# Kernel optimization log

Measured on AMD Instinct MI355X. Metric: run time of the kernel, lower is better.

## Reference

```python
import jax, jax.numpy as jnp
import numpy as np

B, C, H, W = 4, 512, 64, 208
HID = 512          # params.text_hidden_dim; must equal C for view(1,C,H,-1)
DS = 16            # 1/scale_factor for nearest downsample of the mask
N_REG = 4          # four region-indexed attention modules


def setup_inputs() -> dict:
    key = jax.random.key(0)
    ks = jax.random.split(key, 7)
    image_feature = jax.random.normal(ks[0], (B, C, H, W), dtype=jnp.float32)
    text_feat = jax.random.normal(ks[1], (N_REG, B, HID), dtype=jnp.float32)
    # Mask is constant per (full-res) column so that each region's pixel count
    # is divisible by H, as the original view(1, C, H, -1) requires.
    col_labels = jax.random.randint(ks[2], (B, W * DS), 1, N_REG + 1)
    text_mask = jnp.broadcast_to(
        col_labels[:, None, None, :], (B, 1, H * DS, W * DS)
    ).astype(jnp.int32)
    # Per-region MHA params (nn.Linear weights, no bias assumed).
    Wq = jax.random.normal(ks[3], (N_REG, C, HID), dtype=jnp.float32) * (C ** -0.5)
    Wk = jax.random.normal(ks[4], (N_REG, HID, HID), dtype=jnp.float32) * (HID ** -0.5)
    Wv = jax.random.normal(ks[5], (N_REG, HID, HID), dtype=jnp.float32) * (HID ** -0.5)
    Wo = jax.random.normal(ks[6], (N_REG, HID, C), dtype=jnp.float32) * (HID ** -0.5)
    return {
        "image_feature": image_feature,
        "text_feat": text_feat,
        "text_mask": text_mask,
        "Wq": Wq,
        "Wk": Wk,
        "Wv": Wv,
        "Wo": Wo,
    }


def reference(image_feature, text_feat, text_mask, Wq, Wk, Wv, Wo):
    # F.interpolate(scale=1/16, mode='nearest') == strided slicing for integer stride.
    mask_ds = text_mask[:, 0, ::DS, ::DS]          # [B, H, W]
    col_labels = mask_ds[:, 0, :]                  # [B, W] (mask is column-constant)
    # Cross-attention of every region pixel (query) against ONE text token z
    # (single key/value): softmax over a length-1 axis is identically 1, so
    # attn_out = Wo @ (Wv @ z) for every pixel, and Wq/Wk receive zero gradient.
    # With the residual connection: out_pixel = x_pixel + (z Wv) Wo per region.
    delta = jnp.einsum('rbh,rhd,rdc->brc', text_feat, Wv, Wo)          # [B, R, C]
    d_col = jnp.take_along_axis(delta, (col_labels - 1)[:, :, None], axis=1)  # [B, W, C]
    out = image_feature + d_col.transpose(0, 2, 1)[:, :, None, :]      # [B, C, H, W]
    # The torch code concatenates regions along width in sorted-unique label
    # order, i.e. columns are permuted by (label, original column) -- a stable
    # argsort of the column labels.
    order = jnp.argsort(col_labels, axis=1, stable=True)               # [B, W]
    return jnp.take_along_axis(out, order[:, None, None, :], axis=3)
```

## Files before the change

### kernel.cpp

```cpp
#include <hip/hip_runtime.h>

#define B_ 4
#define C_ 512
#define H_ 64
#define W_ 208
#define HID_ 512
#define NREG_ 4
#define DS_ 16


__global__ __launch_bounds__(256) void prepA_kernel(
    const float* __restrict__ tf, const float* __restrict__ Wv,
    const int* __restrict__ mask, float* __restrict__ tmp, int* __restrict__ swl) {
  int blk = blockIdx.x, tid = threadIdx.x;
  if (blk < 256) {
    int r = blk >> 6;
    int h0 = ((blk >> 3) & 7) * 64;
    int d0 = (blk & 7) * 64;
    int g = tid >> 6, dd = tid & 63;
    __shared__ float tf_s[B_][64];
    __shared__ float red[4][B_][64];
    tf_s[g][dd] = tf[(r * B_ + g) * HID_ + h0 + dd];
    __syncthreads();
    float acc[B_] = {};
    for (int hh = g * 16; hh < g * 16 + 16; ++hh) {
      float w = Wv[(size_t)(r * HID_ + h0 + hh) * HID_ + d0 + dd];
#pragma unroll
      for (int b = 0; b < B_; ++b) acc[b] += tf_s[b][hh] * w;
    }
#pragma unroll
    for (int b = 0; b < B_; ++b) red[g][b][dd] = acc[b];
    __syncthreads();
    {
      float s = red[0][g][dd] + red[1][g][dd] + red[2][g][dd] + red[3][g][dd];
      atomicAdd(&tmp[(g * NREG_ + r) * HID_ + d0 + dd], s);
    }
  } else {
    int b = blk - 256;
    const size_t mb = (size_t)b * (H_ * DS_) * (W_ * DS_);
    int w = tid;
    int l = (w < W_) ? (mask[mb + (size_t)w * DS_] - 1) : -1;
    int wave = tid >> 6, lane = tid & 63;
    unsigned long long bal[NREG_];
    __shared__ int wcnt[4][NREG_];
#pragma unroll
    for (int r = 0; r < NREG_; ++r) bal[r] = __ballot(l == r);
    if (lane < NREG_) wcnt[wave][lane] = __popcll(bal[lane]);
    __syncthreads();
    if (w < W_) {
      int pos = 0;
#pragma unroll
      for (int q = 0; q < NREG_; ++q) {
        int tot = wcnt[0][q] + wcnt[1][q] + wcnt[2][q] + wcnt[3][q];
        if (q < l) pos += tot;
      }
#pragma unroll
      for (int v = 0; v < 4; ++v)
        if (v < wave) pos += wcnt[v][l];
      pos += __popcll(bal[l] & ((1ull << lane) - 1ull));
      swl[b * W_ + pos] = w | (l << 16);
    }
  }
}

__global__ __launch_bounds__(256) void prepB_kernel(
    const float* __restrict__ tmp, const float* __restrict__ Wo,
    float* __restrict__ delta) {
  int blk = blockIdx.x, tid = threadIdx.x;
  int r = blk >> 6;
  int d0 = ((blk >> 3) & 7) * 64;
  int c0 = (blk & 7) * 64;
  int g = tid >> 6, cc = tid & 63;
  __shared__ float tmp_s[B_][64];
  __shared__ float red[4][B_][64];
  tmp_s[g][cc] = tmp[(g * NREG_ + r) * HID_ + d0 + cc];
  __syncthreads();
  float acc[B_] = {};
  for (int dd = g * 16; dd < g * 16 + 16; ++dd) {
    float w = Wo[(size_t)(r * HID_ + d0 + dd) * C_ + c0 + cc];
#pragma unroll
    for (int b = 0; b < B_; ++b) acc[b] += tmp_s[b][dd] * w;
  }
#pragma unroll
  for (int b = 0; b < B_; ++b) red[g][b][cc] = acc[b];
  __syncthreads();
  {
    float s = red[0][g][cc] + red[1][g][cc] + red[2][g][cc] + red[3][g][cc];
    atomicAdd(&delta[(g * NREG_ + r) * C_ + c0 + cc], s);
  }
}

#define GITER_ 13
#define RCH_ (W_ / 4)
__global__ void apply_kernel(
    const float* __restrict__ img, const float* __restrict__ delta,
    const int* __restrict__ swl, float* __restrict__ out) {
  int blk = blockIdx.x;
  int b = blk >> 9;
  int c = blk & (C_ - 1);
  int tid = threadIdx.x;
  __shared__ int swl_s[W_];
  __shared__ float dsel_s[NREG_];
  if (tid < W_) swl_s[tid] = swl[b * W_ + tid];
  if (tid < NREG_) dsel_s[tid] = delta[(b * NREG_ + tid) * C_ + c];
  __syncthreads();
  float d0 = dsel_s[0], d1 = dsel_s[1], d2 = dsel_s[2], d3 = dsel_s[3];
  const float* src = img + (size_t)blk * (H_ * W_);
  float4* dst = (float4*)(out + (size_t)blk * (H_ * W_));
  float res[GITER_][4];
#pragma unroll
  for (int g = 0; g < GITER_; ++g) {
    int i = g * 256 + tid;
    int h = i / RCH_;
    int j = i - h * RCH_;
    const float* row = src + h * W_;
#pragma unroll
    for (int k = 0; k < 4; ++k)
      res[g][k] = row[swl_s[j * 4 + k] & 0xFFFF];
  }
#pragma unroll
  for (int g = 0; g < GITER_; ++g) {
    int i = g * 256 + tid;
    int h = i / RCH_;
    int j = i - h * RCH_;
    float4 o;
    float* op = &o.x;
#pragma unroll
    for (int k = 0; k < 4; ++k) {
      int r = swl_s[j * 4 + k] >> 16;
      float dv = (r == 0) ? d0 : (r == 1) ? d1 : (r == 2) ? d2 : d3;
      op[k] = res[g][k] + dv;
    }
    dst[i] = o;
  }
}

extern "C" void kernel_launch(void* const* d_in, const int* in_sizes, int n_in,
                              void* d_out, int out_size, void* d_ws, size_t ws_size,
                              hipStream_t stream) {
  const float* img  = (const float*)d_in[0];
  const float* tf   = (const float*)d_in[1];
  const int*   mask = (const int*)d_in[2];
  const float* Wv   = (const float*)d_in[5];
  const float* Wo   = (const float*)d_in[6];
  float* delta = (float*)d_ws;
  float* tmp   = (float*)((char*)d_ws + 32768);
  int*   swl   = (int*)((char*)d_ws + 65536);
  float* out   = (float*)d_out;

  hipMemsetAsync(d_ws, 0, 65536, stream);
  prepA_kernel<<<260, 256, 0, stream>>>(tf, Wv, mask, tmp, swl);
  prepB_kernel<<<256, 256, 0, stream>>>(tmp, Wo, delta);
  apply_kernel<<<B_ * C_, 256, 0, stream>>>(img, delta, swl, out);
}
```

Before: 237.2 us.

## Stage image rows in LDS for coalesced loads and permute from shared memory

The apply kernel now loads 16-row tiles of the image with coalesced float4 reads, adds a per-column delta that is precomputed into shared memory, writes the result to an LDS tile, and then performs the column permutation as a gather from LDS before coalesced float4 stores. This replaces scattered scalar global gathers and the per-element region select. It adds extra barriers per tile, about 13KB of LDS per block, and a launch-bounds occupancy hint.

```diff
diff --git a/kernel.cpp b/kernel.cpp
--- a/kernel.cpp
+++ b/kernel.cpp
@@ -90,48 +90,64 @@
   }
 }
 
-#define GITER_ 13
 #define RCH_ (W_ / 4)
-__global__ void apply_kernel(
+#define TROWS_ 16
+#define TF4_ (TROWS_ * RCH_)
+__global__ __launch_bounds__(256, 8) void apply_kernel(
     const float* __restrict__ img, const float* __restrict__ delta,
     const int* __restrict__ swl, float* __restrict__ out) {
   int blk = blockIdx.x;
   int b = blk >> 9;
-  int c = blk & (C_ - 1);
   int tid = threadIdx.x;
   __shared__ int swl_s[W_];
+  __shared__ float dval[W_];
   __shared__ float dsel_s[NREG_];
+  __shared__ float tile[TROWS_ * W_];
   if (tid < W_) swl_s[tid] = swl[b * W_ + tid];
-  if (tid < NREG_) dsel_s[tid] = delta[(b * NREG_ + tid) * C_ + c];
+  if (tid < NREG_) dsel_s[tid] = delta[(b * NREG_ + tid) * C_ + (blk & (C_ - 1))];
   __syncthreads();
-  float d0 = dsel_s[0], d1 = dsel_s[1], d2 = dsel_s[2], d3 = dsel_s[3];
-  const float* src = img + (size_t)blk * (H_ * W_);
-  float4* dst = (float4*)(out + (size_t)blk * (H_ * W_));
-  float res[GITER_][4];
+  if (tid < W_) {
+    int e = swl_s[tid];
+    dval[e & 0xFFFF] = dsel_s[e >> 16];
+  }
+  __syncthreads();
+  const float4* srcv = (const float4*)(img + (size_t)blk * (H_ * W_));
+  float4* dstv = (float4*)(out + (size_t)blk * (H_ * W_));
+  const float4* dval4 = (const float4*)dval;
+  const int4* swl4 = (const int4*)swl_s;
+  for (int t = 0; t < H_ / TROWS_; ++t) {
+    int base = t * TF4_;
 #pragma unroll
-  for (int g = 0; g < GITER_; ++g) {
-    int i = g * 256 + tid;
-    int h = i / RCH_;
-    int j = i - h * RCH_;
-    const float* row = src + h * W_;
+    for (int g = 0; g < 4; ++g) {
+      int ii = g * 256 + tid;
+      if (ii < TF4_) {
+        float4 v = srcv[base + ii];
+        int hl = ii / RCH_;
+        int j = ii - hl * RCH_;
+        float4 dv = dval4[j];
+        float4 o;
+        o.x = v.x + dv.x; o.y = v.y + dv.y; o.z = v.z + dv.z; o.w = v.w + dv.w;
+        ((float4*)&tile[hl * W_])[j] = o;
+      }
+    }
+    __syncthreads();
 #pragma unroll
-    for (int k = 0; k < 4; ++k)
-      res[g][k] = row[swl_s[j * 4 + k] & 0xFFFF];
-  }
-#pragma unroll
-  for (int g = 0; g < GITER_; ++g) {
-    int i = g * 256 + tid;
-    int h = i / RCH_;
-    int j = i - h * RCH_;
-    float4 o;
-    float* op = &o.x;
-#pragma unroll
-    for (int k = 0; k < 4; ++k) {
-      int r = swl_s[j * 4 + k] >> 16;
-      float dv = (r == 0) ? d0 : (r == 1) ? d1 : (r == 2) ? d2 : d3;
-      op[k] = res[g][k] + dv;
+    for (int g = 0; g < 4; ++g) {
+      int ii = g * 256 + tid;
+      if (ii < TF4_) {
+        int hl = ii / RCH_;
+        int jo = ii - hl * RCH_;
+        int4 sw = swl4[jo];
+        const float* rowp = &tile[hl * W_];
+        float4 o;
+        o.x = rowp[sw.x & 0xFFFF];
+        o.y = rowp[sw.y & 0xFFFF];
+        o.z = rowp[sw.z & 0xFFFF];
+        o.w = rowp[sw.w & 0xFFFF];
+        dstv[base + ii] = o;
+      }
     }
-    dst[i] = o;
+    __syncthreads();
   }
 }
 
```

Result: slower. 245.3 us (+3.4%).

## Stage image rows in LDS with coalesced float4 loads, drop memset and atomics

Applied to the files above, without the earlier changes.

The apply kernel now has each wave load its 16-row slab of the image with coalesced float4 reads into registers, write it to shared memory, and do the column permutation gather from LDS. This replaces the scattered per-element global reads. Per-column deltas are precomputed into a shared array. The two GEMV prep kernels are restructured so each block covers the full reduction dimension and writes results directly, which removes the memset and the atomicAdds at the cost of fewer, longer-running blocks. The new 53KB LDS tile may limit occupancy in the apply kernel.

```diff
diff --git a/kernel.cpp b/kernel.cpp
--- a/kernel.cpp
+++ b/kernel.cpp
@@ -9,34 +9,42 @@
 #define DS_ 16
 
 
-__global__ __launch_bounds__(256) void prepA_kernel(
+__global__ __launch_bounds__(256) void prep1_kernel(
     const float* __restrict__ tf, const float* __restrict__ Wv,
     const int* __restrict__ mask, float* __restrict__ tmp, int* __restrict__ swl) {
   int blk = blockIdx.x, tid = threadIdx.x;
-  if (blk < 256) {
-    int r = blk >> 6;
-    int h0 = ((blk >> 3) & 7) * 64;
-    int d0 = (blk & 7) * 64;
-    int g = tid >> 6, dd = tid & 63;
-    __shared__ float tf_s[B_][64];
-    __shared__ float red[4][B_][64];
-    tf_s[g][dd] = tf[(r * B_ + g) * HID_ + h0 + dd];
+  if (blk < 64) {
+    int r = blk >> 4;
+    int d0 = (blk & 15) * 32;
+    __shared__ float tf_s[B_ * HID_];
+    __shared__ float red[8][B_][32];
+#pragma unroll
+    for (int k = 0; k < 8; ++k) {
+      int idx = k * 256 + tid;
+      tf_s[idx] = tf[r * (B_ * HID_) + idx];
+    }
     __syncthreads();
+    int hg = tid >> 5, dd = tid & 31;
     float acc[B_] = {};
-    for (int hh = g * 16; hh < g * 16 + 16; ++hh) {
-      float w = Wv[(size_t)(r * HID_ + h0 + hh) * HID_ + d0 + dd];
+#pragma unroll 4
+    for (int q = 0; q < 64; ++q) {
+      int hh = hg * 64 + q;
+      float w = Wv[(size_t)(r * HID_ + hh) * HID_ + d0 + dd];
 #pragma unroll
-      for (int b = 0; b < B_; ++b) acc[b] += tf_s[b][hh] * w;
+      for (int b = 0; b < B_; ++b) acc[b] += tf_s[b * HID_ + hh] * w;
     }
 #pragma unroll
-    for (int b = 0; b < B_; ++b) red[g][b][dd] = acc[b];
+    for (int b = 0; b < B_; ++b) red[hg][b][dd] = acc[b];
     __syncthreads();
-    {
-      float s = red[0][g][dd] + red[1][g][dd] + red[2][g][dd] + red[3][g][dd];
-      atomicAdd(&tmp[(g * NREG_ + r) * HID_ + d0 + dd], s);
+    if (tid < 128) {
+      int b2 = tid >> 5, d2 = tid & 31;
+      float s = 0.f;
+#pragma unroll
+      for (int q = 0; q < 8; ++q) s += red[q][b2][d2];
+      tmp[(b2 * NREG_ + r) * HID_ + d0 + d2] = s;
     }
   } else {
-    int b = blk - 256;
+    int b = blk - 64;
     const size_t mb = (size_t)b * (H_ * DS_) * (W_ * DS_);
     int w = tid;
     int l = (w < W_) ? (mask[mb + (size_t)w * DS_] - 1) : -1;
@@ -63,75 +71,88 @@
   }
 }
 
-__global__ __launch_bounds__(256) void prepB_kernel(
+__global__ __launch_bounds__(256) void prep2_kernel(
     const float* __restrict__ tmp, const float* __restrict__ Wo,
     float* __restrict__ delta) {
   int blk = blockIdx.x, tid = threadIdx.x;
-  int r = blk >> 6;
-  int d0 = ((blk >> 3) & 7) * 64;
+  int r = blk >> 3;
   int c0 = (blk & 7) * 64;
-  int g = tid >> 6, cc = tid & 63;
-  __shared__ float tmp_s[B_][64];
+  __shared__ float tmp_s[B_ * HID_];
   __shared__ float red[4][B_][64];
-  tmp_s[g][cc] = tmp[(g * NREG_ + r) * HID_ + d0 + cc];
+#pragma unroll
+  for (int k = 0; k < 8; ++k) {
+    int idx = k * 256 + tid;
+    int b = idx >> 9, d = idx & 511;
+    tmp_s[idx] = tmp[(b * NREG_ + r) * HID_ + d];
+  }
   __syncthreads();
+  int dg = tid >> 6, cc = tid & 63;
   float acc[B_] = {};
-  for (int dd = g * 16; dd < g * 16 + 16; ++dd) {
-    float w = Wo[(size_t)(r * HID_ + d0 + dd) * C_ + c0 + cc];
+#pragma unroll 4
+  for (int q = 0; q < 128; ++q) {
+    int d = dg * 128 + q;
+    float w = Wo[(size_t)(r * HID_ + d) * C_ + c0 + cc];
 #pragma unroll
-    for (int b = 0; b < B_; ++b) acc[b] += tmp_s[b][dd] * w;
+    for (int b = 0; b < B_; ++b) acc[b] += tmp_s[b * HID_ + d] * w;
   }
 #pragma unroll
-  for (int b = 0; b < B_; ++b) red[g][b][cc] = acc[b];
+  for (int b = 0; b < B_; ++b) red[dg][b][cc] = acc[b];
   __syncthreads();
   {
-    float s = red[0][g][cc] + red[1][g][cc] + red[2][g][cc] + red[3][g][cc];
-    atomicAdd(&delta[(g * NREG_ + r) * C_ + c0 + cc], s);
+    float s = red[0][dg][cc] + red[1][dg][cc] + red[2][dg][cc] + red[3][dg][cc];
+    delta[(dg * NREG_ + r) * C_ + c0 + cc] = s;
   }
 }
 
-#define GITER_ 13
 #define RCH_ (W_ / 4)
-__global__ void apply_kernel(
+__global__ __launch_bounds__(256) void apply_kernel(
     const float* __restrict__ img, const float* __restrict__ delta,
     const int* __restrict__ swl, float* __restrict__ out) {
   int blk = blockIdx.x;
   int b = blk >> 9;
   int c = blk & (C_ - 1);
   int tid = threadIdx.x;
+  int wave = tid >> 6, lane = tid & 63;
   __shared__ int swl_s[W_];
+  __shared__ float dquad[W_];
   __shared__ float dsel_s[NREG_];
+  __shared__ float tile[4][16 * W_];
+
+  const float4* srcv = (const float4*)(img + (size_t)blk * (H_ * W_));
+  float4* dstv = (float4*)(out + (size_t)blk * (H_ * W_));
+  int off = wave * (16 * RCH_);
+
+  float4 pre[13];
+#pragma unroll
+  for (int k = 0; k < 13; ++k) pre[k] = srcv[off + k * 64 + lane];
+
   if (tid < W_) swl_s[tid] = swl[b * W_ + tid];
   if (tid < NREG_) dsel_s[tid] = delta[(b * NREG_ + tid) * C_ + c];
   __syncthreads();
-  float d0 = dsel_s[0], d1 = dsel_s[1], d2 = dsel_s[2], d3 = dsel_s[3];
-  const float* src = img + (size_t)blk * (H_ * W_);
-  float4* dst = (float4*)(out + (size_t)blk * (H_ * W_));
-  float res[GITER_][4];
+  if (tid < W_) dquad[tid] = dsel_s[swl_s[tid] >> 16];
+  __syncthreads();
+
+  float* mytile = &tile[wave][0];
 #pragma unroll
-  for (int g = 0; g < GITER_; ++g) {
-    int i = g * 256 + tid;
-    int h = i / RCH_;
-    int j = i - h * RCH_;
-    const float* row = src + h * W_;
+  for (int k = 0; k < 13; ++k) {
+    ((float4*)mytile)[k * 64 + lane] = pre[k];
+  }
+  const int4* swl4 = (const int4*)swl_s;
+  const float4* dq4 = (const float4*)dquad;
 #pragma unroll
-    for (int k = 0; k < 4; ++k)
-      res[g][k] = row[swl_s[j * 4 + k] & 0xFFFF];
-  }
-#pragma unroll
-  for (int g = 0; g < GITER_; ++g) {
-    int i = g * 256 + tid;
-    int h = i / RCH_;
-    int j = i - h * RCH_;
+  for (int k = 0; k < 13; ++k) {
+    int i = k * 64 + lane;
+    int hl = i / RCH_;
+    int jo = i - hl * RCH_;
+    int4 sw = swl4[jo];
+    float4 dq = dq4[jo];
+    const float* rowp = mytile + hl * W_;
     float4 o;
-    float* op = &o.x;
-#pragma unroll
-    for (int k = 0; k < 4; ++k) {
-      int r = swl_s[j * 4 + k] >> 16;
-      float dv = (r == 0) ? d0 : (r == 1) ? d1 : (r == 2) ? d2 : d3;
-      op[k] = res[g][k] + dv;
-    }
-    dst[i] = o;
+    o.x = rowp[sw.x & 0xFFFF] + dq.x;
+    o.y = rowp[sw.y & 0xFFFF] + dq.y;
+    o.z = rowp[sw.z & 0xFFFF] + dq.z;
+    o.w = rowp[sw.w & 0xFFFF] + dq.w;
+    dstv[off + i] = o;
   }
 }
 
@@ -143,13 +164,12 @@
   const int*   mask = (const int*)d_in[2];
   const float* Wv   = (const float*)d_in[5];
   const float* Wo   = (const float*)d_in[6];
-  float* delta = (float*)d_ws;
-  float* tmp   = (float*)((char*)d_ws + 32768);
+  float* tmp   = (float*)d_ws;
+  float* delta = (float*)((char*)d_ws + 32768);
   int*   swl   = (int*)((char*)d_ws + 65536);
   float* out   = (float*)d_out;
 
-  hipMemsetAsync(d_ws, 0, 65536, stream);
-  prepA_kernel<<<260, 256, 0, stream>>>(tf, Wv, mask, tmp, swl);
-  prepB_kernel<<<256, 256, 0, stream>>>(tmp, Wo, delta);
+  prep1_kernel<<<68, 256, 0, stream>>>(tf, Wv, mask, tmp, swl);
+  prep2_kernel<<<32, 256, 0, stream>>>(tmp, Wo, delta);
   apply_kernel<<<B_ * C_, 256, 0, stream>>>(img, delta, swl, out);
 }
```

New measurement: 277.2 us. 1.17x slower.

## Stage image rows into LDS asynchronously and gather the column permutation from LDS

Applied to the files above, without the earlier changes.

The apply kernel becomes one wave per (batch, channel) plane. It streams 16-row chunks of the plane into a double-buffered LDS tile with global_load_lds, paced by explicit waitcnt instructions so the next chunk loads while the current one is gathered. The permuted column gather and the per-column delta add now read from LDS instead of issuing scattered global loads. Outputs go out as nontemporal vector stores. The cost is low occupancy from about 28 KB of LDS per single-wave block, plus fragile hand-tuned vmcnt counts that depend on how stores are counted.

```diff
diff --git a/kernel.cpp b/kernel.cpp
--- a/kernel.cpp
+++ b/kernel.cpp
@@ -7,6 +7,9 @@
 #define HID_ 512
 #define NREG_ 4
 #define DS_ 16
+
+typedef float f32x4 __attribute__((ext_vector_type(4)));
+typedef int i32x4 __attribute__((ext_vector_type(4)));
 
 
 __global__ __launch_bounds__(256) void prepA_kernel(
@@ -90,49 +93,84 @@
   }
 }
 
-#define GITER_ 13
 #define RCH_ (W_ / 4)
-__global__ void apply_kernel(
+__device__ __forceinline__ void gload_lds16(const float* g, float* l) {
+  __builtin_amdgcn_global_load_lds(
+      (const __attribute__((address_space(1))) void*)g,
+      (__attribute__((address_space(3))) void*)l, 16, 0, 0);
+}
+__global__ __launch_bounds__(64) void apply_kernel(
     const float* __restrict__ img, const float* __restrict__ delta,
     const int* __restrict__ swl, float* __restrict__ out) {
-  int blk = blockIdx.x;
-  int b = blk >> 9;
-  int c = blk & (C_ - 1);
-  int tid = threadIdx.x;
+  int lane = threadIdx.x;
+  int p = blockIdx.x;
+  int b = p >> 9;
+  int c = p & (C_ - 1);
+  __shared__ float tile[2][16 * W_];
   __shared__ int swl_s[W_];
-  __shared__ float dsel_s[NREG_];
-  if (tid < W_) swl_s[tid] = swl[b * W_ + tid];
-  if (tid < NREG_) dsel_s[tid] = delta[(b * NREG_ + tid) * C_ + c];
-  __syncthreads();
-  float d0 = dsel_s[0], d1 = dsel_s[1], d2 = dsel_s[2], d3 = dsel_s[3];
-  const float* src = img + (size_t)blk * (H_ * W_);
-  float4* dst = (float4*)(out + (size_t)blk * (H_ * W_));
-  float res[GITER_][4];
+  __shared__ float dq_s[W_];
+
+  if (lane < 52) ((i32x4*)swl_s)[lane] = ((const i32x4*)(swl + b * W_))[lane];
+  float v0 = 0.f;
+  if (lane < NREG_) v0 = delta[(b * NREG_ + lane) * C_ + c];
+  float e0 = __shfl(v0, 0), e1 = __shfl(v0, 1), e2 = __shfl(v0, 2), e3 = __shfl(v0, 3);
 #pragma unroll
-  for (int g = 0; g < GITER_; ++g) {
-    int i = g * 256 + tid;
-    int h = i / RCH_;
-    int j = i - h * RCH_;
-    const float* row = src + h * W_;
+  for (int q = 0; q < 4; ++q) {
+    int pos = q * 64 + lane;
+    if (pos < W_) {
+      int lab = swl_s[pos] >> 16;
+      dq_s[pos] = lab == 0 ? e0 : lab == 1 ? e1 : lab == 2 ? e2 : e3;
+    }
+  }
+  const float* src = img + (size_t)p * (H_ * W_);
+  f32x4* dstv = (f32x4*)out + (size_t)p * (H_ * RCH_);
+
+  asm volatile("s_waitcnt vmcnt(0)" ::: "memory");
 #pragma unroll
-    for (int k = 0; k < 4; ++k)
-      res[g][k] = row[swl_s[j * 4 + k] & 0xFFFF];
-  }
+  for (int k = 0; k < 13; ++k)
+    gload_lds16(src + (k * 64 + lane) * 4, &tile[0][k * 256]);
 #pragma unroll
-  for (int g = 0; g < GITER_; ++g) {
-    int i = g * 256 + tid;
-    int h = i / RCH_;
-    int j = i - h * RCH_;
-    float4 o;
-    float* op = &o.x;
+  for (int k = 0; k < 13; ++k)
+    gload_lds16(src + 16 * W_ + (k * 64 + lane) * 4, &tile[1][k * 256]);
+
+  const i32x4* swl4 = (const i32x4*)swl_s;
+  const f32x4* dq4 = (const f32x4*)dq_s;
+  auto gather_unit = [&](int u) {
+    const float* mytile = tile[u & 1];
+    f32x4* du = dstv + u * (16 * RCH_);
 #pragma unroll
-    for (int k = 0; k < 4; ++k) {
-      int r = swl_s[j * 4 + k] >> 16;
-      float dv = (r == 0) ? d0 : (r == 1) ? d1 : (r == 2) ? d2 : d3;
-      op[k] = res[g][k] + dv;
+    for (int k = 0; k < 13; ++k) {
+      int i = k * 64 + lane;
+      int hl = i / RCH_;
+      int jo = i - hl * RCH_;
+      i32x4 sw = swl4[jo];
+      f32x4 dq = dq4[jo];
+      const float* rowp = mytile + hl * W_;
+      f32x4 o;
+      o.x = rowp[sw.x & 0xFFFF] + dq.x;
+      o.y = rowp[sw.y & 0xFFFF] + dq.y;
+      o.z = rowp[sw.z & 0xFFFF] + dq.z;
+      o.w = rowp[sw.w & 0xFFFF] + dq.w;
+      __builtin_nontemporal_store(o, &du[i]);
     }
-    dst[i] = o;
-  }
+  };
+
+  asm volatile("s_waitcnt vmcnt(13)" ::: "memory");
+  gather_unit(0);
+  asm volatile("s_waitcnt lgkmcnt(0)" ::: "memory");
+#pragma unroll
+  for (int k = 0; k < 13; ++k)
+    gload_lds16(src + 2 * 16 * W_ + (k * 64 + lane) * 4, &tile[0][k * 256]);
+  asm volatile("s_waitcnt vmcnt(26)" ::: "memory");
+  gather_unit(1);
+  asm volatile("s_waitcnt lgkmcnt(0)" ::: "memory");
+#pragma unroll
+  for (int k = 0; k < 13; ++k)
+    gload_lds16(src + 3 * 16 * W_ + (k * 64 + lane) * 4, &tile[1][k * 256]);
+  asm volatile("s_waitcnt vmcnt(26)" ::: "memory");
+  gather_unit(2);
+  asm volatile("s_waitcnt vmcnt(13)" ::: "memory");
+  gather_unit(3);
 }
 
 extern "C" void kernel_launch(void* const* d_in, const int* in_sizes, int n_in,
@@ -151,5 +189,5 @@
   hipMemsetAsync(d_ws, 0, 65536, stream);
   prepA_kernel<<<260, 256, 0, stream>>>(tf, Wv, mask, tmp, swl);
   prepB_kernel<<<256, 256, 0, stream>>>(tmp, Wo, delta);
-  apply_kernel<<<B_ * C_, 256, 0, stream>>>(img, delta, swl, out);
+  apply_kernel<<<B_ * C_, 64, 0, stream>>>(img, delta, swl, out);
 }
```

New measurement: 246.7 us. +4.0%, slower.
